# Kernel tuning notes

Hardware: AMD Instinct MI355X
Metric: run time of the kernel (lower is better)

Reference implementation:

```python
import jax, jax.numpy as jnp
import numpy as np

C = 256        # channels per FPN level (in_channels == representation_size)
PATCH = 5      # GNN kernel_size == stride
NEG_SLOPE = 0.2
K = 7          # node_connectivities[0]


def _conv1x1(x, w, b):
    return jnp.einsum('bchw,oc->bohw', x, w) + b[None, :, None, None]


def _conv3x3(x, w, b):
    y = jax.lax.conv_general_dilated(x, w, (1, 1), 'SAME',
                                     dimension_numbers=('NCHW', 'OIHW', 'NCHW'))
    return y + b[None, :, None, None]


def _nearest(x, hout, wout):
    hin, win = x.shape[-2:]
    ih = (jnp.arange(hout) * hin) // hout
    iw = (jnp.arange(wout) * win) // wout
    return x[..., ih, :][..., iw]


def _topk_edges(score, k, n):
    # torch: A.scatter(1, topk_idx, topk_val); edge = nonzero(triu(A)); edge=[col,row]
    vals, idx = jax.lax.top_k(score, k)          # per-row top-k
    row = jnp.repeat(jnp.arange(n), k)
    col = idx.reshape(-1)
    val = vals.reshape(-1)
    # triu keeps col>=row; GATv2Conv removes self loops then re-adds one per node
    mask = (col > row) & (val != 0.0)
    loop = jnp.arange(n)
    src = jnp.concatenate([col, loop])           # PyG edge_index[0] = source
    dst = jnp.concatenate([row, loop])
    emask = jnp.concatenate([mask, jnp.ones((n,), bool)])
    return src, dst, emask


def _gatv2(x, src, dst, emask, wl, bl, wr, br, att, bias, n):
    heads, dout = att.shape
    xl = (x @ wl + bl).reshape(n, heads, dout)   # source transform (lin_l)
    xr = (x @ wr + br).reshape(n, heads, dout)   # target transform (lin_r)
    m = xl[src] + xr[dst]                        # [E, H, D]
    e = jnp.sum(jax.nn.leaky_relu(m, NEG_SLOPE) * att[None], axis=-1)  # [E, H]
    e = jnp.where(emask[:, None], e, -1e30)
    emax = jax.ops.segment_max(e, dst, num_segments=n)
    w = jnp.exp(e - emax[dst]) * emask[:, None]
    denom = jax.ops.segment_sum(w, dst, num_segments=n)
    alpha = w / (denom[dst] + 1e-16)
    out = jax.ops.segment_sum(alpha[..., None] * xl[src], dst, num_segments=n)
    return out.reshape(n, heads * dout) + bias


def _gnn(x, p, k):
    # x: [1, C, H, W], H,W divisible by PATCH
    _, c, hh, ww = x.shape
    nh, nw = hh // PATCH, ww // PATCH
    n = nh * nw
    patches = x[0].reshape(c, nh, PATCH, nw, PATCH).transpose(1, 3, 0, 2, 4)
    patches = patches.reshape(n, c, PATCH, PATCH)
    emb = jax.nn.relu(jnp.einsum('ncij,ocij->no', patches, p['conv1_w']) + p['conv1_b'])
    emb = jax.nn.relu(emb @ p['fc2_w'].T + p['fc2_b'])
    # feature-similarity kNN graph
    src, dst, em = _topk_edges(emb @ emb.T, k, n)
    h = jax.nn.elu(_gatv2(emb, src, dst, em, *p['g1'], n))
    h = jax.nn.elu(_gatv2(h, src, dst, em, *p['g2'], n))
    # spatial kNN graph (k smallest distances; self distance 0 drops out via val!=0)
    ii, jj = jnp.meshgrid(jnp.arange(nh) * PATCH, jnp.arange(nw) * PATCH, indexing='ij')
    centers = jnp.stack([ii.reshape(-1), jj.reshape(-1)], -1).astype(x.dtype)
    dist = jnp.sqrt(jnp.sum((centers[:, None] - centers[None]) ** 2, -1))
    src2, dst2, em2 = _topk_edges(-dist, k, n)
    h2 = jax.nn.elu(_gatv2(emb, src2, dst2, em2, *p['g3'], n))
    h2 = jax.nn.elu(_gatv2(h2, src2, dst2, em2, *p['g4'], n))
    hc = jax.nn.relu(jnp.concatenate([h, h2], 1) @ p['fc3_w'].T + p['fc3_b']) + h2
    # torch: reshape(dim,dim,C).swapdims(-1,0) -> [C, nw, nh]
    grid = jnp.transpose(hc.reshape(nh, nw, c), (2, 1, 0))
    # ConvTranspose2d(C, C, 5, stride=5): non-overlapping tiling
    up = jnp.einsum('cij,coab->oiajb', grid, p['convT_w'])
    up = up.reshape(c, nw * PATCH, nh * PATCH) + p['convT_b'][:, None, None]
    return jax.nn.relu(up)[None]


def _forward(feat0, feat1, inner_w, inner_b, layer_w, layer_b, convT_w, convT_b,
             conv1_w, conv1_b, fc2_w, fc2_b, fc3_w, fc3_b,
             g1_wl, g1_bl, g1_wr, g1_br, g1_att, g1_bias,
             g2_wl, g2_bl, g2_wr, g2_br, g2_att, g2_bias,
             g3_wl, g3_bl, g3_wr, g3_br, g3_att, g3_bias,
             g4_wl, g4_bl, g4_wr, g4_br, g4_att, g4_bias, k):
    feats = [feat0, feat1]
    xs = []
    for i, f in enumerate(feats):
        p = dict(conv1_w=conv1_w[i], conv1_b=conv1_b[i],
                 fc2_w=fc2_w[i], fc2_b=fc2_b[i],
                 fc3_w=fc3_w[i], fc3_b=fc3_b[i],
                 convT_w=convT_w[i], convT_b=convT_b[i],
                 g1=(g1_wl[i], g1_bl[i], g1_wr[i], g1_br[i], g1_att[i], g1_bias[i]),
                 g2=(g2_wl[i], g2_bl[i], g2_wr[i], g2_br[i], g2_att[i], g2_bias[i]),
                 g3=(g3_wl[i], g3_bl[i], g3_wr[i], g3_br[i], g3_att[i], g3_bias[i]),
                 g4=(g4_wl[i], g4_bl[i], g4_wr[i], g4_br[i], g4_att[i], g4_bias[i]))
        xs.append(f + _gnn(f, p, k))
    # top-down FPN
    last = _conv1x1(xs[1], inner_w[1], inner_b[1])
    out1 = _conv3x3(last, layer_w[1], layer_b[1])
    inner0 = _conv1x1(xs[0], inner_w[0], inner_b[0])
    td = _nearest(last, xs[0].shape[-2], xs[0].shape[-1])
    out0 = _conv3x3(inner0 + td, layer_w[0], layer_b[0])
    return out0, out1


def setup_inputs() -> dict:
    key = jax.random.key(0)
    keys = jax.random.split(key, 48)
    it = iter(range(48))
    def rn(shape, s=0.05):
        return (jax.random.normal(keys[next(it)], shape) * s).astype(jnp.float32)
    H8 = 8 * C
    inp = dict(
        feat0=rn((1, C, 200, 200), 1.0),
        feat1=rn((1, C, 100, 100), 1.0),
        inner_w=rn((2, C, C)), inner_b=rn((2, C)),
        layer_w=rn((2, C, C, 3, 3)), layer_b=rn((2, C)),
        convT_w=rn((2, C, C, PATCH, PATCH)), convT_b=rn((2, C)),
        conv1_w=rn((2, C, C, PATCH, PATCH)), conv1_b=rn((2, C)),
        fc2_w=rn((2, C, C)), fc2_b=rn((2, C)),
        fc3_w=rn((2, C, 2 * C)), fc3_b=rn((2, C)),
        g1_wl=rn((2, C, H8)), g1_bl=rn((2, H8)), g1_wr=rn((2, C, H8)), g1_br=rn((2, H8)),
        g1_att=rn((2, 8, C)), g1_bias=rn((2, H8)),
        g2_wl=rn((2, H8, C)), g2_bl=rn((2, C)), g2_wr=rn((2, H8, C)), g2_br=rn((2, C)),
        g2_att=rn((2, 1, C)), g2_bias=rn((2, C)),
        g3_wl=rn((2, C, H8)), g3_bl=rn((2, H8)), g3_wr=rn((2, C, H8)), g3_br=rn((2, H8)),
        g3_att=rn((2, 8, C)), g3_bias=rn((2, H8)),
        g4_wl=rn((2, H8, C)), g4_bl=rn((2, C)), g4_wr=rn((2, H8, C)), g4_br=rn((2, C)),
        g4_att=rn((2, 1, C)), g4_bias=rn((2, C)),
        k=K,
    )
    return inp


def reference(feat0, feat1, inner_w, inner_b, layer_w, layer_b, convT_w, convT_b,
              conv1_w, conv1_b, fc2_w, fc2_b, fc3_w, fc3_b,
              g1_wl, g1_bl, g1_wr, g1_br, g1_att, g1_bias,
              g2_wl, g2_bl, g2_wr, g2_br, g2_att, g2_bias,
              g3_wl, g3_bl, g3_wr, g3_br, g3_att, g3_bias,
              g4_wl, g4_bl, g4_wr, g4_br, g4_att, g4_bias, k):
    return _forward(feat0, feat1, inner_w, inner_b, layer_w, layer_b, convT_w, convT_b,
                    conv1_w, conv1_b, fc2_w, fc2_b, fc3_w, fc3_b,
                    g1_wl, g1_bl, g1_wr, g1_br, g1_att, g1_bias,
                    g2_wl, g2_bl, g2_wr, g2_br, g2_att, g2_bias,
                    g3_wl, g3_bl, g3_wr, g3_br, g3_att, g3_bias,
                    g4_wl, g4_bl, g4_wr, g4_br, g4_att, g4_bias, k)
```

## Files before the change

### kernel.cpp

```cpp
#include <hip/hip_runtime.h>
#include <cstdint>
#include <cstddef>
#include <math.h>

#define KNN 7

using short8  = __attribute__((ext_vector_type(8))) short;
using floatx4 = __attribute__((ext_vector_type(4))) float;

static const size_t OFF_ARENA = 0;
static const size_t OFF_XS0   = 10240000;
static const size_t OFF_XS1   = 20480000;
static const size_t OFF_LAST  = 23040000;
static const size_t OFF_EMB   = 25600000;
static const size_t OFF_EMB2  = 26009600;
static const size_t OFF_XL    = 26419200;
static const size_t OFF_H1    = 32972800;
static const size_t OFF_XL2   = 36249600;
static const size_t OFF_CAT   = 37068800;
static const size_t OFF_HC    = 37888000;
static const size_t OFF_SRCF  = 38400000;
static const size_t OFF_SRCS  = 38411200;
static const size_t OFF_BF_A  = 38422400;
static const size_t OFF_BF_W  = 40122400;

static __device__ __forceinline__ unsigned short f2bf(float f) {
    union { float f; unsigned u; } v; v.f = f;
    unsigned u = v.u;
    unsigned r = u + 0x7fffu + ((u >> 16) & 1u);
    return (unsigned short)(r >> 16);
}

static __device__ __forceinline__ float bf2f(unsigned short h) {
    union { unsigned u; float f; } v; v.u = ((unsigned)h) << 16; return v.f;
}

static __device__ __forceinline__ void glds16(const void* g, void* l) {
    __builtin_amdgcn_global_load_lds((const __attribute__((address_space(1))) void*)g,
                                     (__attribute__((address_space(3))) void*)l, 16, 0, 0);
}

template<int ACT, bool BIAS>
__global__ __launch_bounds__(256)
void gemm_k(const float* __restrict__ A, const float* __restrict__ B,
            const float* __restrict__ bias, float* __restrict__ C, int M, int N, int K)
{
    __shared__ float As[16][68];
    __shared__ float Bs[16][68];
    const int tid = threadIdx.x;
    const int bm0 = blockIdx.y * 64;
    const int bn0 = blockIdx.x * 64;
    const int tx = tid & 15, ty = tid >> 4;
    const int lrow = tid >> 2;
    const int lk4  = (tid & 3) << 2;
    const int m = bm0 + lrow;
    const int nn = bn0 + lrow;
    const bool aok = m < M, bok = nn < N;
    float acc[4][4] = {{0.f,0.f,0.f,0.f},{0.f,0.f,0.f,0.f},{0.f,0.f,0.f,0.f},{0.f,0.f,0.f,0.f}};

    float4 va = {0.f,0.f,0.f,0.f}, vb = {0.f,0.f,0.f,0.f};
    if (aok) va = *(const float4*)(A + (size_t)m * K + lk4);
    if (bok) vb = *(const float4*)(B + (size_t)nn * K + lk4);

    for (int k0 = 0; k0 < K; k0 += 16) {
        As[lk4+0][lrow]=va.x; As[lk4+1][lrow]=va.y; As[lk4+2][lrow]=va.z; As[lk4+3][lrow]=va.w;
        Bs[lk4+0][lrow]=vb.x; Bs[lk4+1][lrow]=vb.y; Bs[lk4+2][lrow]=vb.z; Bs[lk4+3][lrow]=vb.w;
        __syncthreads();
        float4 na = {0.f,0.f,0.f,0.f}, nb = {0.f,0.f,0.f,0.f};
        const bool more = (k0 + 16) < K;
        if (more) {
            if (aok) na = *(const float4*)(A + (size_t)m * K + (k0 + 16 + lk4));
            if (bok) nb = *(const float4*)(B + (size_t)nn * K + (k0 + 16 + lk4));
        }
        #pragma unroll
        for (int k = 0; k < 16; k++) {
            const float4 av = *(const float4*)&As[k][ty << 2];
            const float4 bv = *(const float4*)&Bs[k][tx << 2];
            const float a0=av.x,a1=av.y,a2=av.z,a3=av.w;
            const float b0=bv.x,b1=bv.y,b2=bv.z,b3=bv.w;
            acc[0][0]=fmaf(a0,b0,acc[0][0]); acc[0][1]=fmaf(a0,b1,acc[0][1]);
            acc[0][2]=fmaf(a0,b2,acc[0][2]); acc[0][3]=fmaf(a0,b3,acc[0][3]);
            acc[1][0]=fmaf(a1,b0,acc[1][0]); acc[1][1]=fmaf(a1,b1,acc[1][1]);
            acc[1][2]=fmaf(a1,b2,acc[1][2]); acc[1][3]=fmaf(a1,b3,acc[1][3]);
            acc[2][0]=fmaf(a2,b0,acc[2][0]); acc[2][1]=fmaf(a2,b1,acc[2][1]);
            acc[2][2]=fmaf(a2,b2,acc[2][2]); acc[2][3]=fmaf(a2,b3,acc[2][3]);
            acc[3][0]=fmaf(a3,b0,acc[3][0]); acc[3][1]=fmaf(a3,b1,acc[3][1]);
            acc[3][2]=fmaf(a3,b2,acc[3][2]); acc[3][3]=fmaf(a3,b3,acc[3][3]);
        }
        __syncthreads();
        va = na; vb = nb;
    }
    #pragma unroll
    for (int i = 0; i < 4; i++) {
        const int mm = bm0 + (ty << 2) + i;
        if (mm >= M) continue;
        #pragma unroll
        for (int jj = 0; jj < 4; jj++) {
            const int nc = bn0 + (tx << 2) + jj;
            if (nc >= N) continue;
            float v = acc[i][jj];
            if (BIAS) v += bias[nc];
            if (ACT == 1) v = fmaxf(v, 0.f);
            C[(size_t)mm * N + nc] = v;
        }
    }
}

template<int ACT, bool BIAS>
static inline void gemm32(hipStream_t s, const float* A, const float* B, const float* bias,
                          float* C, int M, int N, int K)
{
    dim3 g((N + 63) / 64, (M + 63) / 64);
    gemm_k<ACT, BIAS><<<g, dim3(256), 0, s>>>(A, B, bias, C, M, N, K);
}

enum { BT_NT = 0, BT_CONV2 = 2 };

template<int BT, int ACT, int BAX, bool ADDMAT>
__global__ __launch_bounds__(256)
void bgemm_k(const unsigned short* __restrict__ A, const unsigned short* __restrict__ B,
             const float* __restrict__ bias, const float* __restrict__ bias2, int nsplit,
             const float* __restrict__ Dmat, int Dld,
             float* __restrict__ C, int M, int N, int K, int imH, int imW)
{
    constexpr int LDS_SH = (BT == BT_CONV2) ? 3 * 4096 : 2 * 8192;
    __shared__ unsigned short As[LDS_SH];
    __shared__ unsigned short Bs[LDS_SH];
    const int tid  = threadIdx.x;
    const int lane = tid & 63;
    const int wid  = tid >> 6;
    const int quad = lane >> 4;
    const int l15  = lane & 15;
    const int wy = wid >> 1, wx = wid & 1;

    int bxx = blockIdx.x, byy = blockIdx.y;
    if (gridDim.y == 2) {
        const int nbx = gridDim.x;
        const int nwg = nbx * 2;
        const int hw  = byy * nbx + bxx;
        const int q = nwg >> 3, r = nwg & 7;
        const int x8 = hw & 7, d = hw >> 3;
        const int lg = (x8 < r) ? x8 * (q + 1) + d : r * (q + 1) + (x8 - r) * q + d;
        byy = lg & 1; bxx = lg >> 1;
    }
    const int bm0 = byy * 128;
    const int bn0 = bxx * 128;
// ... 113 lines not shown
        for (int t = 0; t < T2; t++) {
            if (t + 1 < T2) asm volatile("s_waitcnt vmcnt(8) lgkmcnt(0)" ::: "memory");
            else            asm volatile("s_waitcnt vmcnt(0) lgkmcnt(0)" ::: "memory");
            __builtin_amdgcn_s_barrier();
            __builtin_amdgcn_sched_barrier(0);
            compute(t & 1);
            __builtin_amdgcn_s_barrier();
            __builtin_amdgcn_sched_barrier(0);
            if (t + 2 < T2) stage(t & 1, t + 2);
        }
    }

    #pragma unroll
    for (int i = 0; i < 4; i++) {
        #pragma unroll
        for (int r = 0; r < 4; r++) {
            const int m = bm0 + wy * 64 + i * 16 + quad * 4 + r;
            if (m >= M) continue;
            #pragma unroll
            for (int j = 0; j < 4; j++) {
                const int n = bn0 + wx * 64 + j * 16 + l15;
                if (n >= N) continue;
                float v = acc[i][j][r];
                if (bias != nullptr)
                    v += (BAX == 0) ? bias[m] : (n < nsplit ? bias[n] : bias2[n - nsplit]);
                if (ACT == 1) v = fmaxf(v, 0.f);
                if (ADDMAT) v += Dmat[(size_t)m * Dld + n];
                C[(size_t)m * N + n] = v;
            }
        }
    }
}

template<int BT, int ACT, int BAX, bool ADDMAT>
static inline void bgemm(hipStream_t s, const unsigned short* A, const unsigned short* B,
                         const float* bias, const float* bias2, int nsplit,
                         const float* D, int Dld, float* C,
                         int M, int N, int K, int imH = 0, int imW = 0)
{
    dim3 g((N + 127) / 128, (M + 127) / 128);
    bgemm_k<BT, ACT, BAX, ADDMAT><<<g, dim3(256), 0, s>>>(A, B, bias, bias2, nsplit,
                                                          D, Dld, C, M, N, K, imH, imW);
}

__global__ __launch_bounds__(256)
void bgemm_sk_k(const unsigned short* __restrict__ A, const unsigned short* __restrict__ B,
                float* __restrict__ part, int M, int N, int K, int Kc)
{
    __shared__ unsigned short As[2][8192];
    __shared__ unsigned short Bs[2][8192];
    const int tid  = threadIdx.x;
    const int lane = tid & 63;
    const int wid  = tid >> 6;
    const int quad = lane >> 4;
    const int l15  = lane & 15;
    const int l8   = lane >> 3;
    const int wy = wid >> 1, wx = wid & 1;
    const int bm0 = blockIdx.y * 128;
    const int bn0 = blockIdx.x * 128;
    const int kbeg = blockIdx.z * Kc;
    const int kend = (kbeg + Kc < K) ? kbeg + Kc : K;

    floatx4 zero = {0.f, 0.f, 0.f, 0.f};
    floatx4 acc[4][4];
    #pragma unroll
// ... 158 lines not shown
        compute(t & 1);
        __builtin_amdgcn_s_barrier();
        __builtin_amdgcn_sched_barrier(0);
        if (t + 2 < T2) stage(t & 1, t + 2);
    }

    float* P = part + (size_t)blockIdx.z * M * N;
    #pragma unroll
    for (int i = 0; i < 4; i++) {
        #pragma unroll
        for (int r = 0; r < 4; r++) {
            const int m = bm0 + wy * 64 + i * 16 + quad * 4 + r;
            if (m >= M) continue;
            #pragma unroll
            for (int j = 0; j < 4; j++) {
                const int n = bn0 + wx * 64 + j * 16 + l15;
                if (n >= N) continue;
                P[(size_t)m * N + n] = acc[i][j][r];
            }
        }
    }
}

template<int ACT, bool ADDMAT, bool BIAS = true>
__global__ void bsk_reduce_k(const float* __restrict__ part,
                             const float* __restrict__ bias, const float* __restrict__ bias2,
                             int nsplit, const float* __restrict__ Dmat, int Dld,
                             float* __restrict__ C, int MN, int N, int S)
{
    const int i4 = (blockIdx.x * 256 + threadIdx.x) * 4;
    if (i4 >= MN) return;
    float4 a = *(const float4*)(part + i4);
    for (int s = 1; s < S; s++) {
        const float4 b = *(const float4*)(part + (size_t)s * MN + i4);
        a.x += b.x; a.y += b.y; a.z += b.z; a.w += b.w;
    }
    const int n = i4 % N;
    if (BIAS) {
        const float* bb = (n < nsplit) ? (bias + n) : (bias2 + n - nsplit);
        a.x += bb[0]; a.y += bb[1]; a.z += bb[2]; a.w += bb[3];
    }
    if (ACT == 1) {
        a.x = fmaxf(a.x, 0.f); a.y = fmaxf(a.y, 0.f);
        a.z = fmaxf(a.z, 0.f); a.w = fmaxf(a.w, 0.f);
    }
    if (ADDMAT) {
        const int m = i4 / N;
        const float4 d = *(const float4*)(Dmat + (size_t)m * Dld + n);
        a.x += d.x; a.y += d.y; a.z += d.z; a.w += d.w;
    }
    *(float4*)(C + i4) = a;
}

template<int ACT, bool ADDMAT>
static inline void bgemm_sk(hipStream_t s, const unsigned short* A, const unsigned short* B,
                            const float* bias, const float* bias2, int nsplit,
                            const float* D, int Dld, float* C, float* part,
                            int M, int N, int K, int S)
{
    const int Kc = ((K / S + 63) / 64) * 64;
    dim3 g((N + 127) / 128, (M + 127) / 128, S);
    bgemm_sk_k<<<g, dim3(256), 0, s>>>(A, B, part, M, N, K, Kc);
    const int MN = M * N;
    bsk_reduce_k<ACT, ADDMAT><<<dim3((MN / 4 + 255) / 256), dim3(256), 0, s>>>(
        part, bias, bias2, nsplit, D, Dld, C, MN, N, S);
}

__global__ void cast_bf16_k(const float* __restrict__ in, unsigned short* __restrict__ out, int total)
{
    const int i4 = (blockIdx.x * 256 + threadIdx.x) * 4;
    if (i4 + 4 <= total) {
        const float4 v = *(const float4*)(in + i4);
        ushort4 o;
        o.x = f2bf(v.x); o.y = f2bf(v.y); o.z = f2bf(v.z); o.w = f2bf(v.w);
        *(ushort4*)(out + i4) = o;
    } else {
        for (int i = i4; i < total; i++) out[i] = f2bf(in[i]);
    }
}

static inline void cast_bf(hipStream_t s, const float* in, unsigned short* out, int total)
{
    cast_bf16_k<<<dim3((total / 4 + 255) / 256), dim3(256), 0, s>>>(in, out, total);
}

__global__ void cast_hilo_k(const float* __restrict__ in, unsigned short* __restrict__ hi,
                            unsigned short* __restrict__ lo, int total)
{
// ... 59 lines not shown

__global__ void cast_t2_k(const float* __restrict__ in0, const float* __restrict__ in1,
                          unsigned short* __restrict__ out0, unsigned short* __restrict__ out1,
                          int K, int N)
{
    if (blockIdx.z == 0) cast_t_body(in0, out0, K, N);
    else                 cast_t_body(in1, out1, K, N);
}

static inline void cast_t(hipStream_t s, const float* in, unsigned short* out, int K, int N)
{
    cast_t_k<<<dim3((N + 63) / 64, (K + 63) / 64), dim3(256), 0, s>>>(in, out, K, N);
}

static inline void cast_t2(hipStream_t s, const float* in0, const float* in1,
                           unsigned short* out0, unsigned short* out1, int K, int N)
{
    cast_t2_k<<<dim3((N + 63) / 64, (K + 63) / 64, 2), dim3(256), 0, s>>>(in0, in1, out0, out1, K, N);
}

__global__ void cast_t_pad_k(const float* __restrict__ in, const float* __restrict__ up,
                             unsigned short* __restrict__ out, int N, int imW, int upW)
{
    __shared__ float tile[64][65];
    const int n0 = blockIdx.x * 64;
    const int k0 = blockIdx.y * 64;
    const int t = threadIdx.x;
    const int r = t >> 2;
    const int c4 = (t & 3) << 4;
    {
        const int k = k0 + r;
        if (n0 + c4 + 16 <= N) {
            const float4* p = (const float4*)(in + (size_t)k * N + n0 + c4);
            *(float4*)&tile[r][c4]      = p[0];
            *(float4*)&tile[r][c4 + 4]  = p[1];
            *(float4*)&tile[r][c4 + 8]  = p[2];
            *(float4*)&tile[r][c4 + 12] = p[3];
        } else {
            for (int i = 0; i < 16; i++)
                tile[r][c4 + i] = (n0 + c4 + i < N) ? in[(size_t)k * N + n0 + c4 + i] : 0.f;
        }
    }
    __syncthreads();
    const int n = n0 + r;
    if (n >= N) return;
    const int py = n / imW, px = n - py * imW;
    unsigned short tmp[16];
    if (up != nullptr) {
        const float* u = up + (size_t)(py >> 1) * upW + (px >> 1);
        #pragma unroll
        for (int i = 0; i < 16; i++)
            tmp[i] = f2bf(tile[c4 + i][r] + u[(size_t)(k0 + c4 + i) * upW * upW]);
    } else {
        #pragma unroll
        for (int i = 0; i < 16; i++) tmp[i] = f2bf(tile[c4 + i][r]);
    }
    unsigned short* o = out + ((size_t)(py + 1) * (imW + 2) + px + 1) * 256 + k0 + c4;
    *(uint4*)(o)     = *(uint4*)&tmp[0];
    *(uint4*)(o + 8) = *(uint4*)&tmp[8];
}

static inline void cast_t_pad(hipStream_t s, const float* in, const float* up,
                              unsigned short* out, int N, int imW, int upW)
{
    cast_t_pad_k<<<dim3((N + 63) / 64, 4), dim3(256), 0, s>>>(in, up, out, N, imW, upW);
}

__global__ void zero_ring_k(unsigned short* __restrict__ out, int imH, int imW)
{
    const int W2 = imW + 2;
    const int nb = 2 * W2 + 2 * imH;
    const int idx = blockIdx.x * 256 + threadIdx.x;
    if (idx >= nb * 32) return;
    const int p = idx >> 5;
    const int c8 = (idx & 31) << 3;
    int row;
    if (p < W2)            row = p;
    else if (p < 2 * W2)   row = (imH + 1) * W2 + (p - W2);
    else { const int q = p - 2 * W2; const int y = q >> 1;
           row = (y + 1) * W2 + ((q & 1) ? (imW + 1) : 0); }
    *(uint4*)(out + (size_t)row * 256 + c8) = (uint4){0, 0, 0, 0};
}

static inline void zero_ring(hipStream_t s, unsigned short* out, int imH, int imW)
{
    const int tot = (2 * (imW + 2) + 2 * imH) * 32;
    zero_ring_k<<<dim3((tot + 255) / 256), dim3(256), 0, s>>>(out, imH, imW);
}

__global__ void reorder_w3_k(const float* __restrict__ in, unsigned short* __restrict__ out)
{
    const int idx = blockIdx.x * 256 + threadIdx.x;
    if (idx >= 589824) return;
    const int o = idx / 2304;
    const int r = idx - o * 2304;
    const int j = r >> 8;
    const int c = r & 255;
    out[idx] = f2bf(in[(size_t)o * 2304 + c * 9 + j]);
}

__global__ void extract_patches_hilo_k(const float* __restrict__ f,
                                       unsigned short* __restrict__ hi,
                                       unsigned short* __restrict__ lo,
                                       int nw, int H, int total)
{
    int idx = blockIdx.x * 256 + threadIdx.x;
    if (idx >= total) return;
    int q = idx % 6400;
    int p = idx / 6400;
    int c = q / 25;
// ... 62 lines not shown
            if (taken) continue;
            const int ci = c / nw, cj = c - (c / nw) * nw;
            const int dy = (ri - ci) * 5, dx = (rj - cj) * 5;
            const int d2 = dy * dy + dx * dx;
            const int key = (d2 << 11) | c;
            if (key < bkey) bkey = key;
        }
        #pragma unroll
        for (int off = 32; off > 0; off >>= 1) {
            int ok = __shfl_down(bkey, off);
            if (ok < bkey) bkey = ok;
        }
        bkey = __shfl(bkey, 0);
        sel[t] = bkey & 2047;
    }
    if (lane < KNN) {
        int c = -1;
        #pragma unroll
        for (int t = 0; t < KNN; t++) if (lane == t) c = sel[t];
        srcCols[r * KNN + lane] = (c > r) ? c : -1;
    }
}

__global__ void gat_fused_k(const float* __restrict__ x, int xroff, int xstride,
                            const float* __restrict__ att,
                            const int* __restrict__ srcCols, const float* __restrict__ bias,
                            float* __restrict__ out, int n, int H, int ostride, int ooff)
{
    const int wid = (blockIdx.x * blockDim.x + threadIdx.x) >> 6;
    const int lane = threadIdx.x & 63;
    if (wid >= n * H) return;
    const int h = wid % H;
    const int r = wid / H;
    const int d0 = lane << 2;

    const float4 xrf  = *(const float4*)(x + (size_t)r * xstride + xroff + h * 256 + d0);
    const float4 attf = *(const float4*)(att + (size_t)h * 256 + d0);

    int srcs[8];
    #pragma unroll
    for (int s_ = 0; s_ < KNN; s_++) srcs[s_] = srcCols[r * KNN + s_];
    srcs[7] = r;

    float4 xlf[8];
    float  e[8];
    #pragma unroll
    for (int s_ = 0; s_ < 8; s_++) {
        const int c = srcs[s_];
        float4 v = {0.f, 0.f, 0.f, 0.f};
        if (c >= 0) v = *(const float4*)(x + (size_t)c * xstride + h * 256 + d0);
// ... 13 lines not shown
    for (int s_ = 0; s_ < KNN; s_++)
        if (srcs[s_] >= 0) mx = fmaxf(mx, e[s_]);
    float a[8], denom = 0.f;
    #pragma unroll
    for (int s_ = 0; s_ < 8; s_++) {
        a[s_] = (s_ == 7 || srcs[s_] >= 0) ? expf(e[s_] - mx) : 0.f;
        denom += a[s_];
    }
    const float inv = 1.f / (denom + 1e-16f);

    float o0 = 0.f, o1 = 0.f, o2 = 0.f, o3 = 0.f;
    #pragma unroll
    for (int s_ = 0; s_ < 8; s_++) {
        const float al = a[s_] * inv;
        o0 = fmaf(al, xlf[s_].x, o0); o1 = fmaf(al, xlf[s_].y, o1);
        o2 = fmaf(al, xlf[s_].z, o2); o3 = fmaf(al, xlf[s_].w, o3);
    }
    const float* bb = bias + (size_t)h * 256 + d0;
    o0 += bb[0]; o1 += bb[1]; o2 += bb[2]; o3 += bb[3];
    o0 = (o0 > 0.f) ? o0 : (expf(o0) - 1.f);
    o1 = (o1 > 0.f) ? o1 : (expf(o1) - 1.f);
    o2 = (o2 > 0.f) ? o2 : (expf(o2) - 1.f);
    o3 = (o3 > 0.f) ? o3 : (expf(o3) - 1.f);
    float4 res = {o0, o1, o2, o3};
    *(float4*)(out + (size_t)r * ostride + ooff + (size_t)h * 256 + d0) = res;
}

__global__ void scatter_convT_k(const float* __restrict__ f, const float* __restrict__ U,
                                const float* __restrict__ bias, float* __restrict__ xs,
                                int nw, int H, int total)
{
    int idx = blockIdx.x * 256 + threadIdx.x;
    if (idx >= total) return;
    int x = idx % H;
    int t = idx / H;
    int y = t % H;
    int o = t / H;
    int j = y / 5, a = y - j * 5;
    int i = x / 5, b = x - i * 5;
    int p = i * nw + j;
    float v = U[(size_t)p * 6400 + o * 25 + a * 5 + b] + bias[o];
    v = fmaxf(v, 0.f);
    xs[idx] = f[idx] + v;
}

static void run_level(void* const* d_in, float* ws, int l, int H, hipStream_t s)
{
    const float* f = (const float*)d_in[l];
    const int nh = H / 5, nw = nh, n = nh * nw, HW = H * H;

    const float* convT_w = (const float*)d_in[6]  + (size_t)l * 1638400;
    const float* convT_b = (const float*)d_in[7]  + l * 256;
    const float* conv1_w = (const float*)d_in[8]  + (size_t)l * 1638400;
    const float* conv1_b = (const float*)d_in[9]  + l * 256;
    const float* fc2_w   = (const float*)d_in[10] + (size_t)l * 65536;
    const float* fc2_b   = (const float*)d_in[11] + l * 256;
    const float* fc3_w   = (const float*)d_in[12] + (size_t)l * 131072;
    const float* fc3_b   = (const float*)d_in[13] + l * 256;
    const float* g1_wl   = (const float*)d_in[14] + (size_t)l * 524288;
    const float* g1_bl   = (const float*)d_in[15] + l * 2048;
    const float* g1_wr   = (const float*)d_in[16] + (size_t)l * 524288;
    const float* g1_br   = (const float*)d_in[17] + l * 2048;
    const float* g1_att  = (const float*)d_in[18] + l * 2048;
    const float* g1_bias = (const float*)d_in[19] + l * 2048;
    const float* g2_wl   = (const float*)d_in[20] + (size_t)l * 524288;
    const float* g2_bl   = (const float*)d_in[21] + l * 256;
    const float* g2_wr   = (const float*)d_in[22] + (size_t)l * 524288;
    const float* g2_br   = (const float*)d_in[23] + l * 256;
    const float* g2_att  = (const float*)d_in[24] + l * 256;
    const float* g2_bias = (const float*)d_in[25] + l * 256;
    const float* g3_wl   = (const float*)d_in[26] + (size_t)l * 524288;
    const float* g3_bl   = (const float*)d_in[27] + l * 2048;
    const float* g3_wr   = (const float*)d_in[28] + (size_t)l * 524288;
    const float* g3_br   = (const float*)d_in[29] + l * 2048;
    const float* g3_att  = (const float*)d_in[30] + l * 2048;
    const float* g3_bias = (const float*)d_in[31] + l * 2048;
    const float* g4_wl   = (const float*)d_in[32] + (size_t)l * 524288;
    const float* g4_bl   = (const float*)d_in[33] + l * 256;
    const float* g4_wr   = (const float*)d_in[34] + (size_t)l * 524288;
    const float* g4_br   = (const float*)d_in[35] + l * 256;
    const float* g4_att  = (const float*)d_in[36] + l * 256;
    const float* g4_bias = (const float*)d_in[37] + l * 256;

    float* patches = ws + OFF_ARENA;
    float* xs    = ws + (l == 0 ? OFF_XS0 : OFF_XS1);
    float* emb   = ws + OFF_EMB;
    float* emb2  = ws + OFF_EMB2;
    float* score = ws + OFF_LAST;
    float* xlr   = ws + OFF_XL;
    float* h1    = ws + OFF_H1;
    float* xlr2  = ws + OFF_XL2;
    float* cat   = ws + OFF_CAT;
    float* hc    = ws + OFF_HC;
    int* srcF = (int*)(ws + OFF_SRCF);
    int* srcS = (int*)(ws + OFF_SRCS);
    unsigned short* ba = (unsigned short*)(ws + OFF_BF_A);
    unsigned short* bw = (unsigned short*)(ws + OFF_BF_W);
    float* part = ws + OFF_ARENA;

    unsigned short* Ahi = (unsigned short*)(ws + OFF_ARENA);
    unsigned short* Alo = Ahi + (size_t)n * 6400;
    unsigned short* Whi = (unsigned short*)(ws + OFF_BF_A);
    unsigned short* Wlo = Whi + 1638400;
    { int tot = n * 6400;
      extract_patches_hilo_k<<<dim3((tot + 255) / 256), dim3(256), 0, s>>>(f, Ahi, Alo, nw, H, tot); }
    cast_hilo_k<<<dim3((1638400 / 4 + 255) / 256), dim3(256), 0, s>>>(conv1_w, Whi, Wlo, 1638400);
    const int S3 = (l == 0) ? 4 : 8;
    const int Kc1 = ((6400 / S3 + 63) / 64) * 64;
    { dim3 g(2, (n + 127) / 128, 3 * S3);
      bgemm_hilo_sk_k<<<g, dim3(256), 0, s>>>(Ahi, Alo, Whi, Wlo, xlr, n, 256, 6400, Kc1, S3); }
    { const int MN = n * 256;
      bsk_reduce_k<1, false><<<dim3((MN / 4 + 255) / 256), dim3(256), 0, s>>>(
          xlr, conv1_b, conv1_b, 256, nullptr, 0, emb, MN, 256, 3 * S3); }

    gemm32<1, true>(s, emb, fc2_w, fc2_b, emb2, n, 256, 256);

    unsigned short* e2hi = (unsigned short*)(ws + OFF_EMB);
    unsigned short* e2lo = e2hi + (size_t)n * 256;
    cast_hilo_k<<<dim3((n * 256 / 4 + 255) / 256), dim3(256), 0, s>>>(emb2, e2hi, e2lo, n * 256);
    { dim3 g((n + 127) / 128, (n + 127) / 128, 3);
      bgemm_hilo_sk_k<<<g, dim3(256), 0, s>>>(e2hi, e2lo, e2hi, e2lo, part, n, n, 256, 256, 1); }
    { const int MN = n * n;
      bsk_reduce_k<0, false, false><<<dim3((MN / 4 + 255) / 256), dim3(256), 0, s>>>(
          part, nullptr, nullptr, 0, nullptr, 0, score, MN, n, 3); }

    topk_feat_k<<<dim3(n), dim3(64), 0, s>>>(score, srcF, n);
    topk_spatial_k<<<dim3(n), dim3(64), 0, s>>>(srcS, n, nw);

    const int gatw1 = n * 8;
    const int gatw2 = n;

    cast_t2(s, g1_wl, g1_wr, bw, bw + 2048 * 256, 256, 2048);
    if (n >= 1024)
        bgemm<BT_NT, 0, 1, false>(s, e2hi, bw, g1_bl, g1_br, 2048, nullptr, 0, xlr, n, 4096, 256);
    else
        bgemm_sk<0, false>(s, e2hi, bw, g1_bl, g1_br, 2048, nullptr, 0, xlr, part, n, 4096, 256, 2);
    gat_fused_k<<<dim3((gatw1 + 3) / 4), dim3(256), 0, s>>>(xlr, 2048, 4096, g1_att, srcF, g1_bias, h1, n, 8, 2048, 0);

    cast_bf(s, h1, ba, n * 2048);
    cast_t2(s, g2_wl, g2_wr, bw, bw + 256 * 2048, 2048, 256);
    bgemm_sk<0, false>(s, ba, bw, g2_bl, g2_br, 256, nullptr, 0, xlr2, part, n, 512, 2048, 8);
    gat_fused_k<<<dim3((gatw2 + 3) / 4), dim3(256), 0, s>>>(xlr2, 256, 512, g2_att, srcF, g2_bias, cat, n, 1, 512, 0);

    cast_t2(s, g3_wl, g3_wr, bw, bw + 2048 * 256, 256, 2048);
    if (n >= 1024)
        bgemm<BT_NT, 0, 1, false>(s, e2hi, bw, g3_bl, g3_br, 2048, nullptr, 0, xlr, n, 4096, 256);
    else
        bgemm_sk<0, false>(s, e2hi, bw, g3_bl, g3_br, 2048, nullptr, 0, xlr, part, n, 4096, 256, 2);
    gat_fused_k<<<dim3((gatw1 + 3) / 4), dim3(256), 0, s>>>(xlr, 2048, 4096, g3_att, srcS, g3_bias, h1, n, 8, 2048, 0);

    cast_bf(s, h1, ba, n * 2048);
    cast_t2(s, g4_wl, g4_wr, bw, bw + 256 * 2048, 2048, 256);
    bgemm_sk<0, false>(s, ba, bw, g4_bl, g4_br, 256, nullptr, 0, xlr2, part, n, 512, 2048, 8);
    gat_fused_k<<<dim3((gatw2 + 3) / 4), dim3(256), 0, s>>>(xlr2, 256, 512, g4_att, srcS, g4_bias, cat, n, 1, 512, 256);

    cast_bf(s, cat, ba, n * 512);
    cast_bf(s, fc3_w, bw, 131072);
    bgemm_sk<1, true>(s, ba, bw, fc3_b, fc3_b, 256, cat + 256, 512, hc, part, n, 256, 512, 4);
    cast_bf(s, hc, ba, n * 256);
    cast_t(s, convT_w, bw, 256, 6400);
    bgemm<BT_NT, 0, 1, false>(s, ba, bw, nullptr, nullptr, 0, nullptr, 0, patches, n, 6400, 256);
    { int tot = 256 * HW;
      scatter_convT_k<<<dim3((tot + 255) / 256), dim3(256), 0, s>>>(f, patches, convT_b, xs, nw, H, tot); }
}

extern "C" void kernel_launch(void* const* d_in, const int* in_sizes, int n_in,
                              void* d_out, int out_size, void* d_ws, size_t ws_size,
                              hipStream_t stream)
{
    float* ws  = (float*)d_ws;
    float* out = (float*)d_out;

    run_level(d_in, ws, 0, 200, stream);
    run_level(d_in, ws, 1, 100, stream);

    const float* inner_w = (const float*)d_in[2];
    const float* inner_b = (const float*)d_in[3];
    const float* layer_w = (const float*)d_in[4];
    const float* layer_b = (const float*)d_in[5];
    float* xs0    = ws + OFF_XS0;
    float* xs1    = ws + OFF_XS1;
    float* last   = ws + OFF_LAST;
    float* inner0 = ws + OFF_ARENA;
    unsigned short* bimg = (unsigned short*)(ws + OFF_XL);
    unsigned short* bw1  = (unsigned short*)(ws + OFF_BF_W);
    unsigned short* bwc  = (unsigned short*)(ws + OFF_BF_W + 100000);

    cast_t(stream, xs1, bimg, 256, 10000);
    cast_bf(stream, inner_w + 65536, bw1, 65536);
    bgemm<BT_NT, 0, 0, false>(stream, bw1, bimg, inner_b + 256, nullptr, 0, nullptr, 0,
                              last, 256, 10000, 256);
    reorder_w3_k<<<dim3((589824 + 255) / 256), dim3(256), 0, stream>>>(layer_w + 589824, bwc);
    zero_ring(stream, bimg, 100, 100);
    cast_t_pad(stream, last, nullptr, bimg, 10000, 100, 0);
    bgemm<BT_CONV2, 0, 0, false>(stream, bwc, bimg, layer_b + 256, nullptr, 0, nullptr, 0,
                                 out + 10240000, 256, 10000, 2304, 100, 100);

    cast_t(stream, xs0, bimg, 256, 40000);
    cast_bf(stream, inner_w, bw1, 65536);
    bgemm<BT_NT, 0, 0, false>(stream, bw1, bimg, inner_b, nullptr, 0, nullptr, 0,
                              inner0, 256, 40000, 256);
    reorder_w3_k<<<dim3((589824 + 255) / 256), dim3(256), 0, stream>>>(layer_w, bwc);
    zero_ring(stream, bimg, 200, 200);
    cast_t_pad(stream, inner0, last, bimg, 40000, 200, 100);
    bgemm<BT_CONV2, 0, 0, false>(stream, bwc, bimg, layer_b, nullptr, 0, nullptr, 0,
                                 out, 256, 40000, 2304, 200, 200);
}
```

Measured before the change: 1.117 ms.

## Fuse casts, convT scatter and ring zeroing into producer kernels; fc2 via hi/lo bf16 MFMA

Several producer kernels now write bf16 (or hi/lo bf16) outputs directly: the split-K reduce for conv1/fc2/fc3 and the GAT kernels. This removes the separate cast_bf/cast_hilo passes and their fp32 intermediates. The fp32 fc2 GEMM is replaced with the hi/lo bf16 split-K MFMA path. The convT GEMM epilogue now scatters into the image with bias, ReLU and residual add, which drops the patches buffer and the scatter kernel. Ring zeroing is folded into cast_t_pad as an extra grid row, trading a few launches and memory round trips for slightly more complex epilogues and possible uncoalesced scattered stores.

```diff
diff --git a/kernel.cpp b/kernel.cpp
--- a/kernel.cpp
+++ b/kernel.cpp
@@ -40,88 +40,15 @@
                                      (__attribute__((address_space(3))) void*)l, 16, 0, 0);
 }
 
-template<int ACT, bool BIAS>
-__global__ __launch_bounds__(256)
-void gemm_k(const float* __restrict__ A, const float* __restrict__ B,
-            const float* __restrict__ bias, float* __restrict__ C, int M, int N, int K)
-{
-    __shared__ float As[16][68];
-    __shared__ float Bs[16][68];
-    const int tid = threadIdx.x;
-    const int bm0 = blockIdx.y * 64;
-    const int bn0 = blockIdx.x * 64;
-    const int tx = tid & 15, ty = tid >> 4;
-    const int lrow = tid >> 2;
-    const int lk4  = (tid & 3) << 2;
-    const int m = bm0 + lrow;
-    const int nn = bn0 + lrow;
-    const bool aok = m < M, bok = nn < N;
-    float acc[4][4] = {{0.f,0.f,0.f,0.f},{0.f,0.f,0.f,0.f},{0.f,0.f,0.f,0.f},{0.f,0.f,0.f,0.f}};
-
-    float4 va = {0.f,0.f,0.f,0.f}, vb = {0.f,0.f,0.f,0.f};
-    if (aok) va = *(const float4*)(A + (size_t)m * K + lk4);
-    if (bok) vb = *(const float4*)(B + (size_t)nn * K + lk4);
-
-    for (int k0 = 0; k0 < K; k0 += 16) {
-        As[lk4+0][lrow]=va.x; As[lk4+1][lrow]=va.y; As[lk4+2][lrow]=va.z; As[lk4+3][lrow]=va.w;
-        Bs[lk4+0][lrow]=vb.x; Bs[lk4+1][lrow]=vb.y; Bs[lk4+2][lrow]=vb.z; Bs[lk4+3][lrow]=vb.w;
-        __syncthreads();
-        float4 na = {0.f,0.f,0.f,0.f}, nb = {0.f,0.f,0.f,0.f};
-        const bool more = (k0 + 16) < K;
-        if (more) {
-            if (aok) na = *(const float4*)(A + (size_t)m * K + (k0 + 16 + lk4));
-            if (bok) nb = *(const float4*)(B + (size_t)nn * K + (k0 + 16 + lk4));
-        }
-        #pragma unroll
-        for (int k = 0; k < 16; k++) {
-            const float4 av = *(const float4*)&As[k][ty << 2];
-            const float4 bv = *(const float4*)&Bs[k][tx << 2];
-            const float a0=av.x,a1=av.y,a2=av.z,a3=av.w;
-            const float b0=bv.x,b1=bv.y,b2=bv.z,b3=bv.w;
-            acc[0][0]=fmaf(a0,b0,acc[0][0]); acc[0][1]=fmaf(a0,b1,acc[0][1]);
-            acc[0][2]=fmaf(a0,b2,acc[0][2]); acc[0][3]=fmaf(a0,b3,acc[0][3]);
-            acc[1][0]=fmaf(a1,b0,acc[1][0]); acc[1][1]=fmaf(a1,b1,acc[1][1]);
-            acc[1][2]=fmaf(a1,b2,acc[1][2]); acc[1][3]=fmaf(a1,b3,acc[1][3]);
-            acc[2][0]=fmaf(a2,b0,acc[2][0]); acc[2][1]=fmaf(a2,b1,acc[2][1]);
-            acc[2][2]=fmaf(a2,b2,acc[2][2]); acc[2][3]=fmaf(a2,b3,acc[2][3]);
-            acc[3][0]=fmaf(a3,b0,acc[3][0]); acc[3][1]=fmaf(a3,b1,acc[3][1]);
-            acc[3][2]=fmaf(a3,b2,acc[3][2]); acc[3][3]=fmaf(a3,b3,acc[3][3]);
-        }
-        __syncthreads();
-        va = na; vb = nb;
-    }
-    #pragma unroll
-    for (int i = 0; i < 4; i++) {
-        const int mm = bm0 + (ty << 2) + i;
-        if (mm >= M) continue;
-        #pragma unroll
-        for (int jj = 0; jj < 4; jj++) {
-            const int nc = bn0 + (tx << 2) + jj;
-            if (nc >= N) continue;
-            float v = acc[i][jj];
-            if (BIAS) v += bias[nc];
-            if (ACT == 1) v = fmaxf(v, 0.f);
-            C[(size_t)mm * N + nc] = v;
-        }
-    }
-}
-
-template<int ACT, bool BIAS>
-static inline void gemm32(hipStream_t s, const float* A, const float* B, const float* bias,
-                          float* C, int M, int N, int K)
-{
-    dim3 g((N + 63) / 64, (M + 63) / 64);
-    gemm_k<ACT, BIAS><<<g, dim3(256), 0, s>>>(A, B, bias, C, M, N, K);
-}
-
 enum { BT_NT = 0, BT_CONV2 = 2 };
 
-template<int BT, int ACT, int BAX, bool ADDMAT>
+template<int BT, int ACT, int BAX, bool ADDMAT, int EPI>
 __global__ __launch_bounds__(256)
 void bgemm_k(const unsigned short* __restrict__ A, const unsigned short* __restrict__ B,
              const float* __restrict__ bias, const float* __restrict__ bias2, int nsplit,
              const float* __restrict__ Dmat, int Dld,
-             float* __restrict__ C, int M, int N, int K, int imH, int imW)
+             float* __restrict__ C, int M, int N, int K, int imH, int imW,
+             const float* __restrict__ fEP, const float* __restrict__ bEP, int nwEP)
 {
     constexpr int LDS_SH = (BT == BT_CONV2) ? 3 * 4096 : 2 * 8192;
     __shared__ unsigned short As[LDS_SH];
@@ -281,11 +208,22 @@
                 const int n = bn0 + wx * 64 + j * 16 + l15;
                 if (n >= N) continue;
                 float v = acc[i][j][r];
-                if (bias != nullptr)
-                    v += (BAX == 0) ? bias[m] : (n < nsplit ? bias[n] : bias2[n - nsplit]);
-                if (ACT == 1) v = fmaxf(v, 0.f);
-                if (ADDMAT) v += Dmat[(size_t)m * Dld + n];
-                C[(size_t)m * N + n] = v;
+                if (EPI == 1) {
+                    const int o = n / 25;
+                    const int rm = n - o * 25;
+                    const int a2 = rm / 5, b2 = rm - (rm / 5) * 5;
+                    const int mh = m / nwEP, ml = m - (m / nwEP) * nwEP;
+                    const size_t ix = (size_t)o * imH * imH + (size_t)(ml * 5 + a2) * imH
+                                    + mh * 5 + b2;
+                    v = fmaxf(v + bEP[o], 0.f);
+                    C[ix] = fEP[ix] + v;
+                } else {
+                    if (bias != nullptr)
+                        v += (BAX == 0) ? bias[m] : (n < nsplit ? bias[n] : bias2[n - nsplit]);
+                    if (ACT == 1) v = fmaxf(v, 0.f);
+                    if (ADDMAT) v += Dmat[(size_t)m * Dld + n];
+                    C[(size_t)m * N + n] = v;
+                }
             }
         }
     }
@@ -298,8 +236,19 @@
                          int M, int N, int K, int imH = 0, int imW = 0)
 {
     dim3 g((N + 127) / 128, (M + 127) / 128);
-    bgemm_k<BT, ACT, BAX, ADDMAT><<<g, dim3(256), 0, s>>>(A, B, bias, bias2, nsplit,
-                                                          D, Dld, C, M, N, K, imH, imW);
+    bgemm_k<BT, ACT, BAX, ADDMAT, 0><<<g, dim3(256), 0, s>>>(A, B, bias, bias2, nsplit,
+                                                             D, Dld, C, M, N, K, imH, imW,
+                                                             nullptr, nullptr, 0);
+}
+
+static inline void bgemm_convT(hipStream_t s, const unsigned short* A, const unsigned short* B,
+                               const float* f, const float* cb, float* xs,
+                               int M, int nw, int H)
+{
+    dim3 g((6400 + 127) / 128, (M + 127) / 128);
+    bgemm_k<BT_NT, 0, 0, false, 1><<<g, dim3(256), 0, s>>>(A, B, nullptr, nullptr, 0,
+                                                           nullptr, 0, xs, M, 6400, 256, H, 0,
+                                                           f, cb, nw);
 }
 
 __global__ __launch_bounds__(256)
@@ -504,11 +453,13 @@
     }
 }
 
-template<int ACT, bool ADDMAT, bool BIAS = true>
+template<int ACT, bool ADDMAT, bool BIAS, int OUT>
 __global__ void bsk_reduce_k(const float* __restrict__ part,
                              const float* __restrict__ bias, const float* __restrict__ bias2,
                              int nsplit, const float* __restrict__ Dmat, int Dld,
-                             float* __restrict__ C, int MN, int N, int S)
+                             float* __restrict__ C, unsigned short* __restrict__ Chi,
+                             unsigned short* __restrict__ Clo,
+                             int MN, int N, int S)
 {
     const int i4 = (blockIdx.x * 256 + threadIdx.x) * 4;
     if (i4 >= MN) return;
@@ -531,7 +482,21 @@
         const float4 d = *(const float4*)(Dmat + (size_t)m * Dld + n);
         a.x += d.x; a.y += d.y; a.z += d.z; a.w += d.w;
     }
-    *(float4*)(C + i4) = a;
+    if (OUT == 0) {
+        *(float4*)(C + i4) = a;
+    } else if (OUT == 1) {
+        ushort4 h;
+        h.x = f2bf(a.x); h.y = f2bf(a.y); h.z = f2bf(a.z); h.w = f2bf(a.w);
+        *(ushort4*)(Chi + i4) = h;
+    } else {
+        ushort4 h, l;
+        h.x = f2bf(a.x); l.x = f2bf(a.x - bf2f(h.x));
+        h.y = f2bf(a.y); l.y = f2bf(a.y - bf2f(h.y));
+        h.z = f2bf(a.z); l.z = f2bf(a.z - bf2f(h.z));
+        h.w = f2bf(a.w); l.w = f2bf(a.w - bf2f(h.w));
+        *(ushort4*)(Chi + i4) = h;
+        *(ushort4*)(Clo + i4) = l;
+    }
 }
 
 template<int ACT, bool ADDMAT>
@@ -544,8 +509,8 @@
     dim3 g((N + 127) / 128, (M + 127) / 128, S);
     bgemm_sk_k<<<g, dim3(256), 0, s>>>(A, B, part, M, N, K, Kc);
     const int MN = M * N;
-    bsk_reduce_k<ACT, ADDMAT><<<dim3((MN / 4 + 255) / 256), dim3(256), 0, s>>>(
-        part, bias, bias2, nsplit, D, Dld, C, MN, N, S);
+    bsk_reduce_k<ACT, ADDMAT, true, 0><<<dim3((MN / 4 + 255) / 256), dim3(256), 0, s>>>(
+        part, bias, bias2, nsplit, D, Dld, C, nullptr, nullptr, MN, N, S);
 }
 
 __global__ void cast_bf16_k(const float* __restrict__ in, unsigned short* __restrict__ out, int total)
@@ -651,6 +616,22 @@
 __global__ void cast_t_pad_k(const float* __restrict__ in, const float* __restrict__ up,
                              unsigned short* __restrict__ out, int N, int imW, int upW)
 {
+    if (blockIdx.y == 4) {
+        const int imH = N / imW;
+        const int W2 = imW + 2;
+        const int nb = 2 * W2 + 2 * imH;
+        const int idx = blockIdx.x * 256 + threadIdx.x;
+        if (idx >= nb * 32) return;
+        const int p = idx >> 5;
+        const int c8 = (idx & 31) << 3;
+        int row;
+        if (p < W2)            row = p;
+        else if (p < 2 * W2)   row = (imH + 1) * W2 + (p - W2);
+        else { const int q = p - 2 * W2; const int y = q >> 1;
+               row = (y + 1) * W2 + ((q & 1) ? (imW + 1) : 0); }
+        *(uint4*)(out + (size_t)row * 256 + c8) = (uint4){0, 0, 0, 0};
+        return;
+    }
     __shared__ float tile[64][65];
     const int n0 = blockIdx.x * 64;
     const int k0 = blockIdx.y * 64;
@@ -692,29 +673,7 @@
 static inline void cast_t_pad(hipStream_t s, const float* in, const float* up,
                               unsigned short* out, int N, int imW, int upW)
 {
-    cast_t_pad_k<<<dim3((N + 63) / 64, 4), dim3(256), 0, s>>>(in, up, out, N, imW, upW);
-}
-
-__global__ void zero_ring_k(unsigned short* __restrict__ out, int imH, int imW)
-{
-    const int W2 = imW + 2;
-    const int nb = 2 * W2 + 2 * imH;
-    const int idx = blockIdx.x * 256 + threadIdx.x;
-    if (idx >= nb * 32) return;
-    const int p = idx >> 5;
-    const int c8 = (idx & 31) << 3;
-    int row;
-    if (p < W2)            row = p;
-    else if (p < 2 * W2)   row = (imH + 1) * W2 + (p - W2);
-    else { const int q = p - 2 * W2; const int y = q >> 1;
-           row = (y + 1) * W2 + ((q & 1) ? (imW + 1) : 0); }
-    *(uint4*)(out + (size_t)row * 256 + c8) = (uint4){0, 0, 0, 0};
-}
-
-static inline void zero_ring(hipStream_t s, unsigned short* out, int imH, int imW)
-{
-    const int tot = (2 * (imW + 2) + 2 * imH) * 32;
-    zero_ring_k<<<dim3((tot + 255) / 256), dim3(256), 0, s>>>(out, imH, imW);
+    cast_t_pad_k<<<dim3((N + 63) / 64, 5), dim3(256), 0, s>>>(in, up, out, N, imW, upW);
 }
 
 __global__ void reorder_w3_k(const float* __restrict__ in, unsigned short* __restrict__ out)
@@ -823,10 +782,12 @@
     }
 }
 
+template<int OM>
 __global__ void gat_fused_k(const float* __restrict__ x, int xroff, int xstride,
                             const float* __restrict__ att,
                             const int* __restrict__ srcCols, const float* __restrict__ bias,
-                            float* __restrict__ out, int n, int H, int ostride, int ooff)
+                            float* __restrict__ out, unsigned short* __restrict__ outb,
+                            int n, int H, int ostride, int ooff)
 {
     const int wid = (blockIdx.x * blockDim.x + threadIdx.x) >> 6;
     const int lane = threadIdx.x & 63;
@@ -886,32 +847,20 @@
     o1 = (o1 > 0.f) ? o1 : (expf(o1) - 1.f);
     o2 = (o2 > 0.f) ? o2 : (expf(o2) - 1.f);
     o3 = (o3 > 0.f) ? o3 : (expf(o3) - 1.f);
-    float4 res = {o0, o1, o2, o3};
-    *(float4*)(out + (size_t)r * ostride + ooff + (size_t)h * 256 + d0) = res;
-}
-
-__global__ void scatter_convT_k(const float* __restrict__ f, const float* __restrict__ U,
-                                const float* __restrict__ bias, float* __restrict__ xs,
-                                int nw, int H, int total)
-{
-    int idx = blockIdx.x * 256 + threadIdx.x;
-    if (idx >= total) return;
-    int x = idx % H;
-    int t = idx / H;
-    int y = t % H;
-    int o = t / H;
-    int j = y / 5, a = y - j * 5;
-    int i = x / 5, b = x - i * 5;
-    int p = i * nw + j;
-    float v = U[(size_t)p * 6400 + o * 25 + a * 5 + b] + bias[o];
-    v = fmaxf(v, 0.f);
-    xs[idx] = f[idx] + v;
+    const size_t oi = (size_t)r * ostride + ooff + (size_t)h * 256 + d0;
+    if (OM == 2) {
+        float4 res = {o0, o1, o2, o3};
+        *(float4*)(out + oi) = res;
+    }
+    ushort4 rb;
+    rb.x = f2bf(o0); rb.y = f2bf(o1); rb.z = f2bf(o2); rb.w = f2bf(o3);
+    *(ushort4*)(outb + oi) = rb;
 }
 
 static void run_level(void* const* d_in, float* ws, int l, int H, hipStream_t s)
 {
     const float* f = (const float*)d_in[l];
-    const int nh = H / 5, nw = nh, n = nh * nw, HW = H * H;
+    const int nh = H / 5, nw = nh, n = nh * nw;
 
     const float* convT_w = (const float*)d_in[6]  + (size_t)l * 1638400;
     const float* convT_b = (const float*)d_in[7]  + l * 256;
@@ -946,26 +895,28 @@
     const float* g4_att  = (const float*)d_in[36] + l * 256;
     const float* g4_bias = (const float*)d_in[37] + l * 256;
 
-    float* patches = ws + OFF_ARENA;
     float* xs    = ws + (l == 0 ? OFF_XS0 : OFF_XS1);
-    float* emb   = ws + OFF_EMB;
-    float* emb2  = ws + OFF_EMB2;
     float* score = ws + OFF_LAST;
     float* xlr   = ws + OFF_XL;
-    float* h1    = ws + OFF_H1;
     float* xlr2  = ws + OFF_XL2;
     float* cat   = ws + OFF_CAT;
-    float* hc    = ws + OFF_HC;
     int* srcF = (int*)(ws + OFF_SRCF);
     int* srcS = (int*)(ws + OFF_SRCS);
-    unsigned short* ba = (unsigned short*)(ws + OFF_BF_A);
-    unsigned short* bw = (unsigned short*)(ws + OFF_BF_W);
+    unsigned short* bw   = (unsigned short*)(ws + OFF_BF_W);
+    unsigned short* h1b  = (unsigned short*)(ws + OFF_H1);
+    unsigned short* catb = (unsigned short*)(ws + OFF_BF_A);
+    unsigned short* hcb  = (unsigned short*)(ws + OFF_HC);
     float* part = ws + OFF_ARENA;
 
     unsigned short* Ahi = (unsigned short*)(ws + OFF_ARENA);
     unsigned short* Alo = Ahi + (size_t)n * 6400;
     unsigned short* Whi = (unsigned short*)(ws + OFF_BF_A);
     unsigned short* Wlo = Whi + 1638400;
+    unsigned short* embHi = (unsigned short*)(ws + OFF_EMB2);
+    unsigned short* embLo = embHi + (size_t)n * 256;
+    unsigned short* e2hi  = (unsigned short*)(ws + OFF_EMB);
+    unsigned short* e2lo  = e2hi + (size_t)n * 256;
+
     { int tot = n * 6400;
       extract_patches_hilo_k<<<dim3((tot + 255) / 256), dim3(256), 0, s>>>(f, Ahi, Alo, nw, H, tot); }
     cast_hilo_k<<<dim3((1638400 / 4 + 255) / 256), dim3(256), 0, s>>>(conv1_w, Whi, Wlo, 1638400);
@@ -974,19 +925,21 @@
     { dim3 g(2, (n + 127) / 128, 3 * S3);
       bgemm_hilo_sk_k<<<g, dim3(256), 0, s>>>(Ahi, Alo, Whi, Wlo, xlr, n, 256, 6400, Kc1, S3); }
     { const int MN = n * 256;
-      bsk_reduce_k<1, false><<<dim3((MN / 4 + 255) / 256), dim3(256), 0, s>>>(
-          xlr, conv1_b, conv1_b, 256, nullptr, 0, emb, MN, 256, 3 * S3); }
-
-    gemm32<1, true>(s, emb, fc2_w, fc2_b, emb2, n, 256, 256);
-
-    unsigned short* e2hi = (unsigned short*)(ws + OFF_EMB);
-    unsigned short* e2lo = e2hi + (size_t)n * 256;
-    cast_hilo_k<<<dim3((n * 256 / 4 + 255) / 256), dim3(256), 0, s>>>(emb2, e2hi, e2lo, n * 256);
+      bsk_reduce_k<1, false, true, 2><<<dim3((MN / 4 + 255) / 256), dim3(256), 0, s>>>(
+          xlr, conv1_b, conv1_b, 256, nullptr, 0, nullptr, embHi, embLo, MN, 256, 3 * S3); }
+
+    cast_hilo_k<<<dim3((65536 / 4 + 255) / 256), dim3(256), 0, s>>>(fc2_w, bw, bw + 65536, 65536);
+    { dim3 g(2, (n + 127) / 128, 3);
+      bgemm_hilo_sk_k<<<g, dim3(256), 0, s>>>(embHi, embLo, bw, bw + 65536, xlr, n, 256, 256, 256, 1); }
+    { const int MN = n * 256;
+      bsk_reduce_k<1, false, true, 2><<<dim3((MN / 4 + 255) / 256), dim3(256), 0, s>>>(
+          xlr, fc2_b, fc2_b, 256, nullptr, 0, nullptr, e2hi, e2lo, MN, 256, 3); }
+
     { dim3 g((n + 127) / 128, (n + 127) / 128, 3);
       bgemm_hilo_sk_k<<<g, dim3(256), 0, s>>>(e2hi, e2lo, e2hi, e2lo, part, n, n, 256, 256, 1); }
     { const int MN = n * n;
-      bsk_reduce_k<0, false, false><<<dim3((MN / 4 + 255) / 256), dim3(256), 0, s>>>(
-          part, nullptr, nullptr, 0, nullptr, 0, score, MN, n, 3); }
+      bsk_reduce_k<0, false, false, 0><<<dim3((MN / 4 + 255) / 256), dim3(256), 0, s>>>(
+          part, nullptr, nullptr, 0, nullptr, 0, score, nullptr, nullptr, MN, n, 3); }
 
     topk_feat_k<<<dim3(n), dim3(64), 0, s>>>(score, srcF, n);
     topk_spatial_k<<<dim3(n), dim3(64), 0, s>>>(srcS, n, nw);
@@ -999,33 +952,36 @@
         bgemm<BT_NT, 0, 1, false>(s, e2hi, bw, g1_bl, g1_br, 2048, nullptr, 0, xlr, n, 4096, 256);
     else
         bgemm_sk<0, false>(s, e2hi, bw, g1_bl, g1_br, 2048, nullptr, 0, xlr, part, n, 4096, 256, 2);
-    gat_fused_k<<<dim3((gatw1 + 3) / 4), dim3(256), 0, s>>>(xlr, 2048, 4096, g1_att, srcF, g1_bias, h1, n, 8, 2048, 0);
-
-    cast_bf(s, h1, ba, n * 2048);
+    gat_fused_k<1><<<dim3((gatw1 + 3) / 4), dim3(256), 0, s>>>(
+        xlr, 2048, 4096, g1_att, srcF, g1_bias, nullptr, h1b, n, 8, 2048, 0);
+
     cast_t2(s, g2_wl, g2_wr, bw, bw + 256 * 2048, 2048, 256);
-    bgemm_sk<0, false>(s, ba, bw, g2_bl, g2_br, 256, nullptr, 0, xlr2, part, n, 512, 2048, 8);
-    gat_fused_k<<<dim3((gatw2 + 3) / 4), dim3(256), 0, s>>>(xlr2, 256, 512, g2_att, srcF, g2_bias, cat, n, 1, 512, 0);
+    bgemm_sk<0, false>(s, h1b, bw, g2_bl, g2_br, 256, nullptr, 0, xlr2, part, n, 512, 2048, 8);
+    gat_fused_k<2><<<dim3((gatw2 + 3) / 4), dim3(256), 0, s>>>(
+        xlr2, 256, 512, g2_att, srcF, g2_bias, cat, catb, n, 1, 512, 0);
 
     cast_t2(s, g3_wl, g3_wr, bw, bw + 2048 * 256, 256, 2048);
     if (n >= 1024)
         bgemm<BT_NT, 0, 1, false>(s, e2hi, bw, g3_bl, g3_br, 2048, nullptr, 0, xlr, n, 4096, 256);
     else
         bgemm_sk<0, false>(s, e2hi, bw, g3_bl, g3_br, 2048, nullptr, 0, xlr, part, n, 4096, 256, 2);
-    gat_fused_k<<<dim3((gatw1 + 3) / 4), dim3(256), 0, s>>>(xlr, 2048, 4096, g3_att, srcS, g3_bias, h1, n, 8, 2048, 0);
-
-    cast_bf(s, h1, ba, n * 2048);
+    gat_fused_k<1><<<dim3((gatw1 + 3) / 4), dim3(256), 0, s>>>(
+        xlr, 2048, 4096, g3_att, srcS, g3_bias, nullptr, h1b, n, 8, 2048, 0);
+
     cast_t2(s, g4_wl, g4_wr, bw, bw + 256 * 2048, 2048, 256);
-    bgemm_sk<0, false>(s, ba, bw, g4_bl, g4_br, 256, nullptr, 0, xlr2, part, n, 512, 2048, 8);
-    gat_fused_k<<<dim3((gatw2 + 3) / 4), dim3(256), 0, s>>>(xlr2, 256, 512, g4_att, srcS, g4_bias, cat, n, 1, 512, 256);
-
-    cast_bf(s, cat, ba, n * 512);
+    bgemm_sk<0, false>(s, h1b, bw, g4_bl, g4_br, 256, nullptr, 0, xlr2, part, n, 512, 2048, 8);
+    gat_fused_k<2><<<dim3((gatw2 + 3) / 4), dim3(256), 0, s>>>(
+        xlr2, 256, 512, g4_att, srcS, g4_bias, cat, catb, n, 1, 512, 256);
+
     cast_bf(s, fc3_w, bw, 131072);
-    bgemm_sk<1, true>(s, ba, bw, fc3_b, fc3_b, 256, cat + 256, 512, hc, part, n, 256, 512, 4);
-    cast_bf(s, hc, ba, n * 256);
+    { dim3 g(2, (n + 127) / 128, 4);
+      bgemm_sk_k<<<g, dim3(256), 0, s>>>(catb, bw, part, n, 256, 512, 128); }
+    { const int MN = n * 256;
+      bsk_reduce_k<1, true, true, 1><<<dim3((MN / 4 + 255) / 256), dim3(256), 0, s>>>(
+          part, fc3_b, fc3_b, 256, cat + 256, 512, nullptr, hcb, nullptr, MN, 256, 4); }
+
     cast_t(s, convT_w, bw, 256, 6400);
-    bgemm<BT_NT, 0, 1, false>(s, ba, bw, nullptr, nullptr, 0, nullptr, 0, patches, n, 6400, 256);
-    { int tot = 256 * HW;
-      scatter_convT_k<<<dim3((tot + 255) / 256), dim3(256), 0, s>>>(f, patches, convT_b, xs, nw, H, tot); }
+    bgemm_convT(s, hcb, bw, f, convT_b, xs, n, nw, H);
 }
 
 extern "C" void kernel_launch(void* const* d_in, const int* in_sizes, int n_in,
@@ -1055,7 +1011,6 @@
     bgemm<BT_NT, 0, 0, false>(stream, bw1, bimg, inner_b + 256, nullptr, 0, nullptr, 0,
                               last, 256, 10000, 256);
     reorder_w3_k<<<dim3((589824 + 255) / 256), dim3(256), 0, stream>>>(layer_w + 589824, bwc);
-    zero_ring(stream, bimg, 100, 100);
     cast_t_pad(stream, last, nullptr, bimg, 10000, 100, 0);
     bgemm<BT_CONV2, 0, 0, false>(stream, bwc, bimg, layer_b + 256, nullptr, 0, nullptr, 0,
                                  out + 10240000, 256, 10000, 2304, 100, 100);
@@ -1065,7 +1020,6 @@
     bgemm<BT_NT, 0, 0, false>(stream, bw1, bimg, inner_b, nullptr, 0, nullptr, 0,
                               inner0, 256, 40000, 256);
     reorder_w3_k<<<dim3((589824 + 255) / 256), dim3(256), 0, stream>>>(layer_w, bwc);
-    zero_ring(stream, bimg, 200, 200);
     cast_t_pad(stream, inner0, last, bimg, 40000, 200, 100);
     bgemm<BT_CONV2, 0, 0, false>(stream, bwc, bimg, layer_b, nullptr, 0, nullptr, 0,
                                  out, 256, 40000, 2304, 200, 200);
```

Measured after the change: 1.101 ms. About the same (-1.4%).
